# Performance work log

Measured on AMD Instinct MI355X. Metric: run time of the kernel, lower is better.

Reference implementation:

```python
import jax, jax.numpy as jnp
import numpy as np
import math

B = 50        # graphs per batch
NPG = 2000    # nodes per graph
EPG = 12000   # edges per graph
F_IN = 256
NHID = 128
RATIO = 0.8


def setup_inputs() -> dict:
    key = jax.random.key(0)
    ks = jax.random.split(key, 12)
    N = B * NPG
    src_loc = jax.random.randint(ks[0], (B, EPG), 0, NPG)
    dst_loc = jax.random.randint(ks[1], (B, EPG), 0, NPG)
    off = (jnp.arange(B) * NPG)[:, None]
    edge_index = jnp.stack([(src_loc + off).reshape(-1), (dst_loc + off).reshape(-1)]).astype(jnp.int32)

    def lin(k, fi, fo):
        return (jax.random.normal(k, (fi, fo), jnp.float32) / np.sqrt(fi).astype(np.float32))

    return {
        "x": jax.random.normal(ks[2], (N, F_IN), jnp.float32),
        "W1": lin(ks[3], F_IN, NHID), "b1": jnp.zeros(NHID, jnp.float32),
        "Ws1": lin(ks[4], NHID, 1), "bs1": jnp.zeros(1, jnp.float32),
        "W2": lin(ks[5], NHID, NHID), "b2": jnp.zeros(NHID, jnp.float32),
        "Ws2": lin(ks[6], NHID, 1), "bs2": jnp.zeros(1, jnp.float32),
        "W3": lin(ks[7], NHID, NHID), "b3": jnp.zeros(NHID, jnp.float32),
        "Ws3": lin(ks[8], NHID, 1), "bs3": jnp.zeros(1, jnp.float32),
        "Wl": lin(ks[9], 2 * NHID, NHID), "bl": jnp.zeros(NHID, jnp.float32),
        "edge_index": edge_index,
    }


def gcn_conv(x, W, b, src, dst, w, N):
    # PyG GCNConv: D^{-1/2} (A + I) D^{-1/2} X W + b, deg from edge weights + self loop
    h = x @ W
    deg = jax.ops.segment_sum(w, dst, num_segments=N) + 1.0
    dis = jax.lax.rsqrt(deg)
    norm = w * dis[src] * dis[dst]                       # [E]
    agg = jax.ops.segment_sum(h[src] * norm[:, None], dst, num_segments=N)
    return agg + h / deg[:, None] + b                    # self-loop norm = 1/deg


def sag_pool(x, src, dst, w, Ws, bs, n_per_graph):
    N = x.shape[0]
    k = math.ceil(RATIO * n_per_graph)
    score = gcn_conv(x, Ws, bs, src, dst, w, N)[:, 0]    # [N]
    _, topi = jax.lax.top_k(score.reshape(B, n_per_graph), k)
    perm = (topi + (jnp.arange(B) * n_per_graph)[:, None]).reshape(-1)
    x_new = x[perm] * jnp.tanh(score[perm])[:, None]
    # filter_adj: keep edges whose endpoints survive, reindex; dropped edges -> weight 0
    mapping = jnp.full((N,), -1, jnp.int32).at[perm].set(jnp.arange(B * k, dtype=jnp.int32))
    ns, nd = mapping[src], mapping[dst]
    valid = (ns >= 0) & (nd >= 0) & (w > 0)
    return (x_new, jnp.where(valid, ns, 0), jnp.where(valid, nd, 0),
            jnp.where(valid, w, jnp.zeros((), x.dtype)), k)


def readout(x, n):
    # global max pool || global mean pool (equal-size graphs, nodes grouped per graph)
    xr = x.reshape(B, n, -1)
    return jnp.concatenate([xr.max(axis=1), xr.mean(axis=1)], axis=-1)


def reference(x, W1, b1, Ws1, bs1, W2, b2, Ws2, bs2, W3, b3, Ws3, bs3, Wl, bl, edge_index):
    src, dst = edge_index[0], edge_index[1]
    w = jnp.ones(src.shape[0], x.dtype)
    n = NPG
    x = jax.nn.relu(gcn_conv(x, W1, b1, src, dst, w, B * n))
    x, src, dst, w, n = sag_pool(x, src, dst, w, Ws1, bs1, n)
    x1 = readout(x, n)
    x = jax.nn.relu(gcn_conv(x, W2, b2, src, dst, w, B * n))
    x, src, dst, w, n = sag_pool(x, src, dst, w, Ws2, bs2, n)
    x2 = readout(x, n)
    x = jax.nn.relu(gcn_conv(x, W3, b3, src, dst, w, B * n))
    x, src, dst, w, n = sag_pool(x, src, dst, w, Ws3, bs3, n)
    x3 = readout(x, n)
    return jax.nn.relu((x1 + x2 + x3) @ Wl + bl)
```

## Files before the change

kernel.cpp:

```cpp
#include <hip/hip_runtime.h>
#include <math.h>

#define B_GRAPHS 50
#define NPG0     2000
#define EPG      12000
#define F_IN_C   256
#define NHID     128
#define N0       (B_GRAPHS * NPG0)
#define NE       (B_GRAPHS * EPG)
#define RSEG     16
#define GSLOTS   7
#define CPAD     136

typedef _Float16 f16x8 __attribute__((ext_vector_type(8)));
typedef float    f32x4 __attribute__((ext_vector_type(4)));

static inline int cdiv(int a, int b) { return (a + b - 1) / b; }

__global__ void k_fill_start(int* __restrict__ cnt, float* __restrict__ accum) {
    int i = blockIdx.x * 256 + threadIdx.x;
    if (i < N0) cnt[i] = 0;
    if (i < B_GRAPHS * 256) accum[i] = 0.f;
}

__global__ void k_init_edges(const int* __restrict__ ei, int* __restrict__ esrc,
                             int* __restrict__ edst, float* __restrict__ ew,
                             int* __restrict__ cnt) {
    int e = blockIdx.x * 256 + threadIdx.x;
    if (e < NE) {
        int d = ei[NE + e];
        esrc[e] = ei[e]; edst[e] = d; ew[e] = 1.0f;
        atomicAdd(&cnt[d], 1);
    }
}

__global__ void k_cvt_all(const float* __restrict__ W1, const float* __restrict__ W2,
                          const float* __restrict__ W3, _Float16* __restrict__ WT1,
                          _Float16* __restrict__ WT2, _Float16* __restrict__ WT3) {
    int t = blockIdx.x * 256 + threadIdx.x;
    if (t < 128 * 256) {
        int n = t >> 8, kk = t & 255;
        WT1[t] = (_Float16)W1[kk * 128 + n];
    } else if (t < 128 * 256 + 128 * 128) {
        int u = t - 32768; int n = u >> 7, kk = u & 127;
        WT2[u] = (_Float16)W2[kk * 128 + n];
    } else {
        int u = t - 49152; int n = u >> 7, kk = u & 127;
        WT3[u] = (_Float16)W3[kk * 128 + n];
    }
}

template<int FP32IN, int F, int GATHER>
__global__ __launch_bounds__(256) void k_gemm_ws(const void* __restrict__ Xin,
                                                 const _Float16* __restrict__ WT,
                                                 const int* __restrict__ perm,
                                                 const float* __restrict__ gate,
                                                 _Float16* __restrict__ H, int N) {
    constexpr int KH  = (F > 128) ? 128 : F;
    constexpr int K8H = KH / 8;
    constexpr int SMEMSZ = (128 * KH > 128 * CPAD) ? 128 * KH : 128 * CPAD;
    __shared__ _Float16 smem[SMEMSZ];
    const int tid  = threadIdx.x;
    const int wave = tid >> 6, lane = tid & 63;
    const int quad = lane >> 4, l16 = lane & 15;
    const int m_blk = blockIdx.x * 128;

    f32x4 acc[2][8];
#pragma unroll
    for (int i = 0; i < 2; ++i)
#pragma unroll
        for (int j = 0; j < 8; ++j) acc[i][j] = {0.f, 0.f, 0.f, 0.f};

    int row0 = m_blk + wave * 32 + l16;
    int row1 = row0 + 16;
    if (row0 > N - 1) row0 = N - 1;
    if (row1 > N - 1) row1 = N - 1;
    _Float16 g0 = (_Float16)1.0f, g1 = (_Float16)1.0f;
    if (GATHER) {
        g0 = (_Float16)gate[row0]; g1 = (_Float16)gate[row1];
        row0 = perm[row0]; row1 = perm[row1];
    }
    const int sx = l16 & 7;
    constexpr int NKQ = F / 32;

    if (FP32IN) {
        constexpr int PD = (NKQ < 4) ? NKQ : 4;
        const float* base0 = (const float*)Xin + (size_t)row0 * F + quad * 8;
        const float* base1 = (const float*)Xin + (size_t)row1 * F + quad * 8;
        float4 p0[PD][2], p1[PD][2];
#pragma unroll
        for (int i = 0; i < PD; ++i) {
            p0[i][0] = ((const float4*)(base0 + i * 32))[0];
            p0[i][1] = ((const float4*)(base0 + i * 32))[1];
            p1[i][0] = ((const float4*)(base1 + i * 32))[0];
            p1[i][1] = ((const float4*)(base1 + i * 32))[1];
        }
#pragma unroll
        for (int c = tid; c < 128 * K8H; c += 256) {
            int n = c / K8H, k8 = c - n * K8H;
            f16x8 v = *(const f16x8*)&WT[(size_t)(n * (F / 8) + k8) * 8];
            *(f16x8*)&smem[n * KH + ((k8 ^ (n & 7)) << 3)] = v;
        }
        __syncthreads();
#pragma unroll
        for (int kq = 0; kq < NKQ; ++kq) {
            if (KH < F && kq == NKQ / 2) {
                __syncthreads();
#pragma unroll
                for (int c = tid; c < 128 * K8H; c += 256) {
                    int n = c / K8H, k8 = c - n * K8H;
                    f16x8 v = *(const f16x8*)&WT[(size_t)(n * (F / 8) + K8H + k8) * 8];
                    *(f16x8*)&smem[n * KH + ((k8 ^ (n & 7)) << 3)] = v;
                }
                __syncthreads();
            }
            const int b = kq % PD;
            float4 f0 = p0[b][0], f1 = p0[b][1], h0 = p1[b][0], h1 = p1[b][1];
            if (kq + PD < NKQ) {
                p0[b][0] = ((const float4*)(base0 + (kq + PD) * 32))[0];
                p0[b][1] = ((const float4*)(base0 + (kq + PD) * 32))[1];
                p1[b][0] = ((const float4*)(base1 + (kq + PD) * 32))[0];
                p1[b][1] = ((const float4*)(base1 + (kq + PD) * 32))[1];
            }
            f16x8 af0 = (f16x8){(_Float16)f0.x,(_Float16)f0.y,(_Float16)f0.z,(_Float16)f0.w,
                                (_Float16)f1.x,(_Float16)f1.y,(_Float16)f1.z,(_Float16)f1.w};
            f16x8 af1 = (f16x8){(_Float16)h0.x,(_Float16)h0.y,(_Float16)h0.z,(_Float16)h0.w,
                                (_Float16)h1.x,(_Float16)h1.y,(_Float16)h1.z,(_Float16)h1.w};
            f16x8 bf[8];
#pragma unroll
            for (int j = 0; j < 8; ++j)
                bf[j] = *(const f16x8*)&smem[(j * 16 + l16) * KH + (((((kq & 3) << 2) + quad) ^ sx) << 3)];
#pragma unroll
            for (int j = 0; j < 8; ++j) {
                acc[0][j] = __builtin_amdgcn_mfma_f32_16x16x32_f16(af0, bf[j], acc[0][j], 0, 0, 0);
                acc[1][j] = __builtin_amdgcn_mfma_f32_16x16x32_f16(af1, bf[j], acc[1][j], 0, 0, 0);
            }
        }
    } else {
#pragma unroll
        for (int c = tid; c < 128 * K8H; c += 256) {
            int n = c / K8H, k8 = c - n * K8H;
            f16x8 v = *(const f16x8*)&WT[(size_t)(n * K8H + k8) * 8];
            *(f16x8*)&smem[n * KH + ((k8 ^ (n & 7)) << 3)] = v;
        }
        const _Float16* base0 = (const _Float16*)Xin + (size_t)row0 * F + quad * 8;
        const _Float16* base1 = (const _Float16*)Xin + (size_t)row1 * F + quad * 8;
        f16x8 q0[NKQ], q1[NKQ];
#pragma unroll
        for (int i = 0; i < NKQ; ++i) {
            q0[i] = *(const f16x8*)(base0 + i * 32);
            q1[i] = *(const f16x8*)(base1 + i * 32);
        }
        __syncthreads();
#pragma unroll
        for (int kq = 0; kq < NKQ; ++kq) {
            f16x8 af0 = q0[kq], af1 = q1[kq];
            if (GATHER) { af0 = af0 * g0; af1 = af1 * g1; }
            f16x8 bf[8];
#pragma unroll
            for (int j = 0; j < 8; ++j)
                bf[j] = *(const f16x8*)&smem[(j * 16 + l16) * KH + (((((kq & 3) << 2) + quad) ^ sx) << 3)];
#pragma unroll
            for (int j = 0; j < 8; ++j) {
                acc[0][j] = __builtin_amdgcn_mfma_f32_16x16x32_f16(af0, bf[j], acc[0][j], 0, 0, 0);
                acc[1][j] = __builtin_amdgcn_mfma_f32_16x16x32_f16(af1, bf[j], acc[1][j], 0, 0, 0);
            }
        }
    }
    __syncthreads();

    _Float16* sC = smem;
    const int rw = wave * 32;
#pragma unroll
    for (int i = 0; i < 2; ++i)
#pragma unroll
        for (int j = 0; j < 8; ++j)
#pragma unroll
            for (int g = 0; g < 4; ++g)
                sC[(rw + i * 16 + quad * 4 + g) * CPAD + j * 16 + l16] = (_Float16)acc[i][j][g];
    __syncthreads();
    {
        int rr = tid >> 1;
        int gr = m_blk + rr;
        if (gr < N) {
            _Float16* Hr = H + (size_t)gr * 128 + (tid & 1) * 64;
            const _Float16* Sr = sC + rr * CPAD + (tid & 1) * 64;
#pragma unroll
            for (int c = 0; c < 8; ++c)
                *(f16x8*)&Hr[c * 8] = *(const f16x8*)&Sr[c * 8];
        }
    }
}

__global__ __launch_bounds__(256) void k_scan(const int* __restrict__ cnt,
                                              int* __restrict__ offs,
                                              int* __restrict__ cursor, int npg) {
    __shared__ int ch[256];
    int b = blockIdx.x, tid = threadIdx.x;
    int per = (npg + 255) >> 8;
    int base = b * npg;
    int s0 = tid * per;
    int s1 = s0 + per; if (s1 > npg) s1 = npg; if (s0 > npg) s0 = npg;
    int s = 0;
    for (int i = s0; i < s1; ++i) s += cnt[base + i];
    ch[tid] = s;
    __syncthreads();
    for (int d = 1; d < 256; d <<= 1) {
        int t = ch[tid] + ((tid >= d) ? ch[tid - d] : 0);
        __syncthreads();
        ch[tid] = t;
        __syncthreads();
    }
    int run = b * EPG + ch[tid] - s;
    for (int i = s0; i < s1; ++i) {
        offs[base + i] = run; cursor[base + i] = run;
        run += cnt[base + i];
    }
}

__global__ void k_fill_csr(const int* __restrict__ esrc, const int* __restrict__ edst,
                           const float* __restrict__ ew, const int* __restrict__ cnt,
                           int* __restrict__ cursor, int* __restrict__ csr_src,
                           float* __restrict__ csr_norm) {
    int e = blockIdx.x * 256 + threadIdx.x;
    if (e < NE) {
        if (ew[e] > 0.f) {
            int sN = esrc[e], d = edst[e];
            int pos = atomicAdd(&cursor[d], 1);
            csr_src[pos] = sN;
            csr_norm[pos] = rsqrtf((float)(cnt[sN] + 1)) * rsqrtf((float)(cnt[d] + 1));
        }
    }
}

__global__ __launch_bounds__(256) void k_agg(const _Float16* __restrict__ H,
                                             const int* __restrict__ csr_src,
                                             const float* __restrict__ csr_norm,
                                             const int* __restrict__ offs,
                                             const int* __restrict__ cnt,
                                             const float* __restrict__ bias,
                                             const float* __restrict__ Ws,
                                             _Float16* __restrict__ X,
                                             float* __restrict__ hs,
                                             int bpg, int npg) {
    int bi = blockIdx.x;
    int x = bi & 7, s = bi >> 3;
    int gslot = s / bpg, blk = s - gslot * bpg;
    int g = x + 8 * gslot;
    if (g >= B_GRAPHS) return;
    int node = g * npg + blk * 4 + (threadIdx.x >> 6);
    int lane = threadIdx.x & 63;
    int quad = lane >> 4, l16 = lane & 15;

    int st = offs[node], c = cnt[node], en = st + c;
    float acc[8];
#pragma unroll
    for (int j = 0; j < 8; ++j) acc[j] = 0.f;

    if (c > 0) {
        for (int e0 = st; e0 < en; e0 += 8) {
            int eA = e0 + quad, eB = eA + 4;
            int ecA = eA < en ? eA : en - 1;
            int ecB = eB < en ? eB : en - 1;
            int uA = csr_src[ecA], uB = csr_src[ecB];
            float nA = (eA < en) ? csr_norm[ecA] : 0.f;
            float nB = (eB < en) ? csr_norm[ecB] : 0.f;
            f16x8 hA = *(const f16x8*)&H[(size_t)uA * NHID + l16 * 8];
            f16x8 hB = *(const f16x8*)&H[(size_t)uB * NHID + l16 * 8];
#pragma unroll
            for (int j = 0; j < 8; ++j) acc[j] = fmaf((float)hA[j], nA, acc[j]);
#pragma unroll
            for (int j = 0; j < 8; ++j) acc[j] = fmaf((float)hB[j], nB, acc[j]);
        }
    }
#pragma unroll
    for (int j = 0; j < 8; ++j) {
        acc[j] += __shfl_xor(acc[j], 16, 64);
        acc[j] += __shfl_xor(acc[j], 32, 64);
    }
    float invd = 1.f / (float)(c + 1);
    f16x8 hn = *(const f16x8*)&H[(size_t)node * NHID + l16 * 8];
    float4 b0 = *(const float4*)&bias[l16 * 8];
    float4 b1 = *(const float4*)&bias[l16 * 8 + 4];
    float4 w0 = *(const float4*)&Ws[l16 * 8];
    float4 w1 = *(const float4*)&Ws[l16 * 8 + 4];
    const float bb[8] = {b0.x, b0.y, b0.z, b0.w, b1.x, b1.y, b1.z, b1.w};
    const float ww[8] = {w0.x, w0.y, w0.z, w0.w, w1.x, w1.y, w1.z, w1.w};
    float sd = 0.f;
    f16x8 o;
#pragma unroll
    for (int j = 0; j < 8; ++j) {
        float v = fmaxf(acc[j] + (float)hn[j] * invd + bb[j], 0.f);
        o[j] = (_Float16)v;
        sd = fmaf(v, ww[j], sd);
    }
    if (quad == 0)
        *(f16x8*)&X[(size_t)node * NHID + l16 * 8] = o;
    sd += __shfl_xor(sd, 1, 64);
    sd += __shfl_xor(sd, 2, 64);
    sd += __shfl_xor(sd, 4, 64);
    sd += __shfl_xor(sd, 8, 64);
    if (lane == 0) hs[node] = sd;
}

__global__ void k_score(const float* __restrict__ hs, const int* __restrict__ csr_src,
                        const float* __restrict__ csr_norm, const int* __restrict__ offs,
                        const int* __restrict__ cnt, const float* __restrict__ bs,
                        float* __restrict__ score, int N) {
    int i = blockIdx.x * 256 + threadIdx.x;
    if (i >= N) return;
    int s = offs[i], c = cnt[i];
    float a = 0.f;
    for (int e = s; e < s + c; ++e) a = fmaf(hs[csr_src[e]], csr_norm[e], a);
    score[i] = a + hs[i] / (float)(c + 1) + bs[0];
}

__global__ __launch_bounds__(1024) void k_topk(const float* __restrict__ score,
                                               int* __restrict__ mapping,
                                               int* __restrict__ perm,
                                               float* __restrict__ gate,
                                               int* __restrict__ cntN,
                                               int npg, int k) {
    __shared__ float ss[2048];
    __shared__ int   si[2048];
    int b = blockIdx.x, tid = threadIdx.x;
    for (int i = tid; i < 2048; i += 1024) {
        if (i < npg) { ss[i] = score[b * npg + i]; si[i] = i; }
        else         { ss[i] = -__builtin_inff();  si[i] = i; }
    }
    __syncthreads();
    for (int size = 2; size <= 2048; size <<= 1) {
        for (int stride = size >> 1; stride > 0; stride >>= 1) {
            int t = tid;
            int i = ((t & ~(stride - 1)) << 1) | (t & (stride - 1));
            int j = i | stride;
            float sa = ss[i], sb = ss[j];
            int   ia = si[i], ib = si[j];
            bool b_before_a = (sb > sa) || (sb == sa && ib < ia);
            bool forward = ((i & size) == 0);
            bool doswap = forward ? b_before_a : !b_before_a;
            if (doswap) { ss[i] = sb; ss[j] = sa; si[i] = ib; si[j] = ia; }
            __syncthreads();
        }
    }
    for (int j = tid; j < npg; j += 1024) {
        int oldg = b * npg + si[j];
        if (j < k) {
            int newg = b * k + j;
            perm[newg] = oldg;
            mapping[oldg] = newg;
            gate[newg] = tanhf(ss[j]);
        } else {
            mapping[oldg] = -1;
        }
    }
    for (int j = tid; j < k; j += 1024) cntN[b * k + j] = 0;
}

__global__ __launch_bounds__(128) void k_pool_readout(const _Float16* __restrict__ X,
                                                      const float* __restrict__ gate,
                                                      const int* __restrict__ perm,
                                                      float* __restrict__ pmax,
                                                      float* __restrict__ psum, int k) {
    int s = blockIdx.x, b = blockIdx.y, f = threadIdx.x;
    int j0 = (k * s) / RSEG, j1 = (k * (s + 1)) / RSEG;
    float mx = -__builtin_inff(), sm = 0.f;
    for (int j = j0; j < j1; ++j) {
        int g = b * k + j;
        int old = perm[g];
        float v = (float)X[(size_t)old * NHID + f] * gate[g];
        mx = fmaxf(mx, v);
        sm += v;
    }
    pmax[(size_t)(b * RSEG + s) * NHID + f] = mx;
    psum[(size_t)(b * RSEG + s) * NHID + f] = sm;
}

__global__ __launch_bounds__(128) void k_readout_comb(const float* __restrict__ pmax,
                                                      const float* __restrict__ psum,
                                                      float* __restrict__ accum, int k) {
    int b = blockIdx.x, f = threadIdx.x;
    float mx = -__builtin_inff(), sm = 0.f;
#pragma unroll
    for (int s = 0; s < RSEG; ++s) {
        mx = fmaxf(mx, pmax[(size_t)(b * RSEG + s) * NHID + f]);
        sm += psum[(size_t)(b * RSEG + s) * NHID + f];
    }
    accum[b * 256 + f]       += mx;
    accum[b * 256 + 128 + f] += sm / (float)k;
}

__global__ void k_remap(int* __restrict__ esrc, int* __restrict__ edst,
                        float* __restrict__ ew, const int* __restrict__ mapping,
                        int* __restrict__ cntN) {
    int e = blockIdx.x * 256 + threadIdx.x;
    if (e >= NE) return;
    int sN = esrc[e], d = edst[e];
    float we = ew[e];
    int ns = mapping[sN], nd = mapping[d];
    bool valid = (ns >= 0) && (nd >= 0) && (we > 0.f);
    esrc[e] = valid ? ns : 0;
    edst[e] = valid ? nd : 0;
    ew[e] = valid ? we : 0.f;
    if (valid) atomicAdd(&cntN[nd], 1);
}

__global__ __launch_bounds__(128) void k_comb_final(const float* __restrict__ pmax,
                                                    const float* __restrict__ psum,
                                                    const float* __restrict__ accum,
                                                    const float* __restrict__ Wl,
                                                    const float* __restrict__ bl,
                                                    float* __restrict__ out, int k) {
    __shared__ float a[256];
    int b = blockIdx.x, f = threadIdx.x;
    float mx = -__builtin_inff(), sm = 0.f;
#pragma unroll
    for (int s = 0; s < RSEG; ++s) {
        mx = fmaxf(mx, pmax[(size_t)(b * RSEG + s) * NHID + f]);
        sm += psum[(size_t)(b * RSEG + s) * NHID + f];
    }
    a[f]       = accum[b * 256 + f] + mx;
    a[128 + f] = accum[b * 256 + 128 + f] + sm / (float)k;
    __syncthreads();
    float s = bl[f];
    for (int i = 0; i < 256; ++i) s = fmaf(a[i], Wl[i * NHID + f], s);
    out[b * NHID + f] = fmaxf(s, 0.f);
}

extern "C" void kernel_launch(void* const* d_in, const int* in_sizes, int n_in,
                              void* d_out, int out_size, void* d_ws, size_t ws_size,
                              hipStream_t stream) {
    const float* x0 = (const float*)d_in[0];
    const float* Wm[3] = {(const float*)d_in[1], (const float*)d_in[5], (const float*)d_in[9]};
    const float* bm[3] = {(const float*)d_in[2], (const float*)d_in[6], (const float*)d_in[10]};
    const float* Wsc[3] = {(const float*)d_in[3], (const float*)d_in[7], (const float*)d_in[11]};
    const float* bsc[3] = {(const float*)d_in[4], (const float*)d_in[8], (const float*)d_in[12]};
    const float* Wl = (const float*)d_in[13];
    const float* bl = (const float*)d_in[14];
    const int*   ei = (const int*)d_in[15];
    float* out = (float*)d_out;

    _Float16* bufA = (_Float16*)d_ws;
    _Float16* bufB = bufA + (size_t)N0 * NHID;
    _Float16* WT1  = bufB + (size_t)N0 * NHID;
    _Float16* WT2  = WT1 + 128 * 256;
    _Float16* WT3  = WT2 + 128 * 128;
    float* hs     = (float*)(WT3 + 128 * 128);
    float* score  = hs + N0;
    float* gate   = score + N0;
    float* accum  = gate + N0;
    float* pmax   = accum + B_GRAPHS * 256;
    float* psum   = pmax + B_GRAPHS * RSEG * NHID;
    int*   cntA   = (int*)(psum + B_GRAPHS * RSEG * NHID);
    int*   cntB   = cntA + N0;
    int*   offs   = cntB + N0;
    int*   cursor = offs + N0;
    int*   mapping= cursor + N0;
    int*   perm   = mapping + N0;
    int*   esrc   = perm + N0;
    int*   edst   = esrc + NE;
    float* ew     = (float*)(edst + NE);
    int*   csr_src= (int*)(ew + NE);
    float* csr_norm = (float*)(csr_src + NE);

    _Float16* WTs[3] = {WT1, WT2, WT3};
    const int EG = cdiv(NE, 256);

    k_fill_start<<<cdiv(N0, 256), 256, 0, stream>>>(cntA, accum);
    k_init_edges<<<EG, 256, 0, stream>>>(ei, esrc, edst, ew, cntA);
    k_cvt_all<<<256, 256, 0, stream>>>(Wm[0], Wm[1], Wm[2], WT1, WT2, WT3);

    int npg = NPG0;
    _Float16* Hbuf = bufA; _Float16* Xbuf = bufB;

    for (int layer = 0; layer < 3; ++layer) {
        int N = B_GRAPHS * npg;
        int k = (npg * 4) / 5;
        int NG = cdiv(N, 256);
        int bpg = npg >> 2;
        int* cnt  = (layer == 1) ? cntB : cntA;
        int* cntN = (layer == 1) ? cntA : cntB;

        if (layer == 0)
            k_gemm_ws<1, 256, 0><<<cdiv(N, 128), 256, 0, stream>>>(x0, WTs[0], perm, gate, Hbuf, N);
        else
            k_gemm_ws<0, 128, 1><<<cdiv(N, 128), 256, 0, stream>>>(Xbuf, WTs[layer], perm, gate, Hbuf, N);
        k_scan<<<B_GRAPHS, 256, 0, stream>>>(cnt, offs, cursor, npg);
        k_fill_csr<<<EG, 256, 0, stream>>>(esrc, edst, ew, cnt, cursor, csr_src, csr_norm);
        k_agg<<<8 * GSLOTS * bpg, 256, 0, stream>>>(Hbuf, csr_src, csr_norm, offs, cnt,
                                                    bm[layer], Wsc[layer], Xbuf, hs, bpg, npg);
        k_score<<<NG, 256, 0, stream>>>(hs, csr_src, csr_norm, offs, cnt, bsc[layer], score, N);
        k_topk<<<B_GRAPHS, 1024, 0, stream>>>(score, mapping, perm, gate, cntN, npg, k);
        k_pool_readout<<<dim3(RSEG, B_GRAPHS), 128, 0, stream>>>(Xbuf, gate, perm, pmax, psum, k);
        if (layer < 2) {
            k_remap<<<EG, 256, 0, stream>>>(esrc, edst, ew, mapping, cntN);
            k_readout_comb<<<B_GRAPHS, 128, 0, stream>>>(pmax, psum, accum, k);
        } else {
            k_comb_final<<<B_GRAPHS, 128, 0, stream>>>(pmax, psum, accum, Wl, bl, out, k);
        }

        npg = k;
    }
}
```

Before: 639.7 us.

## Halve GEMM row tile, merge init kernels, and fuse readout into one kernel

The GEMM tile shrinks from 128 to 64 rows per block, with one 16-row MFMA strip per wave, which doubles the grid and lowers register pressure to raise occupancy. The edge-init and weight-conversion kernels are merged into a single launch. The two-pass pool readout (partial max/sum, then combine) becomes one 512-thread kernel per graph that reduces in shared memory and, on the last layer, also applies the final linear layer. This removes several launches and the partial buffers, but the readout now runs on only 50 blocks and each GEMM block reuses its loaded weights over fewer rows.

```diff
diff --git a/kernel.cpp b/kernel.cpp
--- a/kernel.cpp
+++ b/kernel.cpp
@@ -8,7 +8,6 @@
 #define NHID     128
 #define N0       (B_GRAPHS * NPG0)
 #define NE       (B_GRAPHS * EPG)
-#define RSEG     16
 #define GSLOTS   7
 #define CPAD     136
 
@@ -23,28 +22,25 @@
     if (i < B_GRAPHS * 256) accum[i] = 0.f;
 }
 
-__global__ void k_init_edges(const int* __restrict__ ei, int* __restrict__ esrc,
-                             int* __restrict__ edst, float* __restrict__ ew,
-                             int* __restrict__ cnt) {
-    int e = blockIdx.x * 256 + threadIdx.x;
-    if (e < NE) {
-        int d = ei[NE + e];
-        esrc[e] = ei[e]; edst[e] = d; ew[e] = 1.0f;
+__global__ void k_init_cvt(const int* __restrict__ ei, int* __restrict__ esrc,
+                           int* __restrict__ edst, float* __restrict__ ew,
+                           int* __restrict__ cnt,
+                           const float* __restrict__ W1, const float* __restrict__ W2,
+                           const float* __restrict__ W3, _Float16* __restrict__ WT1,
+                           _Float16* __restrict__ WT2, _Float16* __restrict__ WT3) {
+    int t = blockIdx.x * 256 + threadIdx.x;
+    if (t < NE) {
+        int d = ei[NE + t];
+        esrc[t] = ei[t]; edst[t] = d; ew[t] = 1.0f;
         atomicAdd(&cnt[d], 1);
     }
-}
-
-__global__ void k_cvt_all(const float* __restrict__ W1, const float* __restrict__ W2,
-                          const float* __restrict__ W3, _Float16* __restrict__ WT1,
-                          _Float16* __restrict__ WT2, _Float16* __restrict__ WT3) {
-    int t = blockIdx.x * 256 + threadIdx.x;
     if (t < 128 * 256) {
         int n = t >> 8, kk = t & 255;
         WT1[t] = (_Float16)W1[kk * 128 + n];
     } else if (t < 128 * 256 + 128 * 128) {
         int u = t - 32768; int n = u >> 7, kk = u & 127;
         WT2[u] = (_Float16)W2[kk * 128 + n];
-    } else {
+    } else if (t < 128 * 256 + 2 * 128 * 128) {
         int u = t - 49152; int n = u >> 7, kk = u & 127;
         WT3[u] = (_Float16)W3[kk * 128 + n];
     }
@@ -58,27 +54,23 @@
                                                  _Float16* __restrict__ H, int N) {
     constexpr int KH  = (F > 128) ? 128 : F;
     constexpr int K8H = KH / 8;
-    constexpr int SMEMSZ = (128 * KH > 128 * CPAD) ? 128 * KH : 128 * CPAD;
+    constexpr int SMEMSZ = (128 * KH > 64 * CPAD) ? 128 * KH : 64 * CPAD;
     __shared__ _Float16 smem[SMEMSZ];
     const int tid  = threadIdx.x;
     const int wave = tid >> 6, lane = tid & 63;
     const int quad = lane >> 4, l16 = lane & 15;
-    const int m_blk = blockIdx.x * 128;
-
-    f32x4 acc[2][8];
-#pragma unroll
-    for (int i = 0; i < 2; ++i)
-#pragma unroll
-        for (int j = 0; j < 8; ++j) acc[i][j] = {0.f, 0.f, 0.f, 0.f};
-
-    int row0 = m_blk + wave * 32 + l16;
-    int row1 = row0 + 16;
+    const int m_blk = blockIdx.x * 64;
+
+    f32x4 acc[8];
+#pragma unroll
+    for (int j = 0; j < 8; ++j) acc[j] = {0.f, 0.f, 0.f, 0.f};
+
+    int row0 = m_blk + wave * 16 + l16;
     if (row0 > N - 1) row0 = N - 1;
-    if (row1 > N - 1) row1 = N - 1;
-    _Float16 g0 = (_Float16)1.0f, g1 = (_Float16)1.0f;
+    _Float16 g0 = (_Float16)1.0f;
     if (GATHER) {
-        g0 = (_Float16)gate[row0]; g1 = (_Float16)gate[row1];
-        row0 = perm[row0]; row1 = perm[row1];
+        g0 = (_Float16)gate[row0];
+        row0 = perm[row0];
     }
     const int sx = l16 & 7;
     constexpr int NKQ = F / 32;
@@ -86,14 +78,11 @@
     if (FP32IN) {
         constexpr int PD = (NKQ < 4) ? NKQ : 4;
         const float* base0 = (const float*)Xin + (size_t)row0 * F + quad * 8;
-        const float* base1 = (const float*)Xin + (size_t)row1 * F + quad * 8;
-        float4 p0[PD][2], p1[PD][2];
+        float4 p0[PD][2];
 #pragma unroll
         for (int i = 0; i < PD; ++i) {
             p0[i][0] = ((const float4*)(base0 + i * 32))[0];
             p0[i][1] = ((const float4*)(base0 + i * 32))[1];
-            p1[i][0] = ((const float4*)(base1 + i * 32))[0];
-            p1[i][1] = ((const float4*)(base1 + i * 32))[1];
         }
 #pragma unroll
         for (int c = tid; c < 128 * K8H; c += 256) {
@@ -115,26 +104,20 @@
                 __syncthreads();
             }
             const int b = kq % PD;
-            float4 f0 = p0[b][0], f1 = p0[b][1], h0 = p1[b][0], h1 = p1[b][1];
+            float4 f0 = p0[b][0], f1 = p0[b][1];
             if (kq + PD < NKQ) {
                 p0[b][0] = ((const float4*)(base0 + (kq + PD) * 32))[0];
                 p0[b][1] = ((const float4*)(base0 + (kq + PD) * 32))[1];
-                p1[b][0] = ((const float4*)(base1 + (kq + PD) * 32))[0];
-                p1[b][1] = ((const float4*)(base1 + (kq + PD) * 32))[1];
             }
             f16x8 af0 = (f16x8){(_Float16)f0.x,(_Float16)f0.y,(_Float16)f0.z,(_Float16)f0.w,
                                 (_Float16)f1.x,(_Float16)f1.y,(_Float16)f1.z,(_Float16)f1.w};
-            f16x8 af1 = (f16x8){(_Float16)h0.x,(_Float16)h0.y,(_Float16)h0.z,(_Float16)h0.w,
-                                (_Float16)h1.x,(_Float16)h1.y,(_Float16)h1.z,(_Float16)h1.w};
             f16x8 bf[8];
 #pragma unroll
             for (int j = 0; j < 8; ++j)
                 bf[j] = *(const f16x8*)&smem[(j * 16 + l16) * KH + (((((kq & 3) << 2) + quad) ^ sx) << 3)];
 #pragma unroll
-            for (int j = 0; j < 8; ++j) {
-                acc[0][j] = __builtin_amdgcn_mfma_f32_16x16x32_f16(af0, bf[j], acc[0][j], 0, 0, 0);
-                acc[1][j] = __builtin_amdgcn_mfma_f32_16x16x32_f16(af1, bf[j], acc[1][j], 0, 0, 0);
-            }
+            for (int j = 0; j < 8; ++j)
+                acc[j] = __builtin_amdgcn_mfma_f32_16x16x32_f16(af0, bf[j], acc[j], 0, 0, 0);
         }
     } else {
 #pragma unroll
@@ -144,49 +127,43 @@
             *(f16x8*)&smem[n * KH + ((k8 ^ (n & 7)) << 3)] = v;
         }
         const _Float16* base0 = (const _Float16*)Xin + (size_t)row0 * F + quad * 8;
-        const _Float16* base1 = (const _Float16*)Xin + (size_t)row1 * F + quad * 8;
-        f16x8 q0[NKQ], q1[NKQ];
-#pragma unroll
-        for (int i = 0; i < NKQ; ++i) {
+        f16x8 q0[NKQ];
+#pragma unroll
+        for (int i = 0; i < NKQ; ++i)
             q0[i] = *(const f16x8*)(base0 + i * 32);
-            q1[i] = *(const f16x8*)(base1 + i * 32);
-        }
         __syncthreads();
 #pragma unroll
         for (int kq = 0; kq < NKQ; ++kq) {
-            f16x8 af0 = q0[kq], af1 = q1[kq];
-            if (GATHER) { af0 = af0 * g0; af1 = af1 * g1; }
+            f16x8 af0 = q0[kq];
+            if (GATHER) af0 = af0 * g0;
             f16x8 bf[8];
 #pragma unroll
             for (int j = 0; j < 8; ++j)
                 bf[j] = *(const f16x8*)&smem[(j * 16 + l16) * KH + (((((kq & 3) << 2) + quad) ^ sx) << 3)];
 #pragma unroll
-            for (int j = 0; j < 8; ++j) {
-                acc[0][j] = __builtin_amdgcn_mfma_f32_16x16x32_f16(af0, bf[j], acc[0][j], 0, 0, 0);
-                acc[1][j] = __builtin_amdgcn_mfma_f32_16x16x32_f16(af1, bf[j], acc[1][j], 0, 0, 0);
-            }
+            for (int j = 0; j < 8; ++j)
+                acc[j] = __builtin_amdgcn_mfma_f32_16x16x32_f16(af0, bf[j], acc[j], 0, 0, 0);
         }
     }
     __syncthreads();
 
     _Float16* sC = smem;
-    const int rw = wave * 32;
-#pragma unroll
-    for (int i = 0; i < 2; ++i)
-#pragma unroll
-        for (int j = 0; j < 8; ++j)
-#pragma unroll
-            for (int g = 0; g < 4; ++g)
-                sC[(rw + i * 16 + quad * 4 + g) * CPAD + j * 16 + l16] = (_Float16)acc[i][j][g];
+    const int rw = wave * 16;
+#pragma unroll
+    for (int j = 0; j < 8; ++j)
+#pragma unroll
+        for (int g = 0; g < 4; ++g)
+            sC[(rw + quad * 4 + g) * CPAD + j * 16 + l16] = (_Float16)acc[j][g];
     __syncthreads();
     {
-        int rr = tid >> 1;
+        int rr = tid >> 2;
+        int cc = (tid & 3) * 32;
         int gr = m_blk + rr;
         if (gr < N) {
-            _Float16* Hr = H + (size_t)gr * 128 + (tid & 1) * 64;
-            const _Float16* Sr = sC + rr * CPAD + (tid & 1) * 64;
-#pragma unroll
-            for (int c = 0; c < 8; ++c)
+            _Float16* Hr = H + (size_t)gr * 128 + cc;
+            const _Float16* Sr = sC + rr * CPAD + cc;
+#pragma unroll
+            for (int c = 0; c < 4; ++c)
                 *(f16x8*)&Hr[c * 8] = *(const f16x8*)&Sr[c * 8];
         }
     }
@@ -357,37 +334,51 @@
     for (int j = tid; j < k; j += 1024) cntN[b * k + j] = 0;
 }
 
-__global__ __launch_bounds__(128) void k_pool_readout(const _Float16* __restrict__ X,
-                                                      const float* __restrict__ gate,
-                                                      const int* __restrict__ perm,
-                                                      float* __restrict__ pmax,
-                                                      float* __restrict__ psum, int k) {
-    int s = blockIdx.x, b = blockIdx.y, f = threadIdx.x;
-    int j0 = (k * s) / RSEG, j1 = (k * (s + 1)) / RSEG;
+template<int FINAL>
+__global__ __launch_bounds__(512) void k_readout(const _Float16* __restrict__ X,
+                                                 const float* __restrict__ gate,
+                                                 const int* __restrict__ perm,
+                                                 float* __restrict__ accum,
+                                                 const float* __restrict__ Wl,
+                                                 const float* __restrict__ bl,
+                                                 float* __restrict__ out, int k) {
+    __shared__ float sred[8][128];
+    __shared__ float afin[256];
+    int b = blockIdx.x;
+    int f = threadIdx.x & 127, seg = threadIdx.x >> 7;
+    int q = k >> 2;
     float mx = -__builtin_inff(), sm = 0.f;
-    for (int j = j0; j < j1; ++j) {
-        int g = b * k + j;
-        int old = perm[g];
-        float v = (float)X[(size_t)old * NHID + f] * gate[g];
+    int g0 = b * k + seg * q;
+    for (int j = 0; j < q; ++j) {
+        int g = g0 + j;
+        float v = (float)X[(size_t)perm[g] * NHID + f] * gate[g];
         mx = fmaxf(mx, v);
         sm += v;
     }
-    pmax[(size_t)(b * RSEG + s) * NHID + f] = mx;
-    psum[(size_t)(b * RSEG + s) * NHID + f] = sm;
-}
-
-__global__ __launch_bounds__(128) void k_readout_comb(const float* __restrict__ pmax,
-                                                      const float* __restrict__ psum,
-                                                      float* __restrict__ accum, int k) {
-    int b = blockIdx.x, f = threadIdx.x;
-    float mx = -__builtin_inff(), sm = 0.f;
-#pragma unroll
-    for (int s = 0; s < RSEG; ++s) {
-        mx = fmaxf(mx, pmax[(size_t)(b * RSEG + s) * NHID + f]);
-        sm += psum[(size_t)(b * RSEG + s) * NHID + f];
-    }
-    accum[b * 256 + f]       += mx;
-    accum[b * 256 + 128 + f] += sm / (float)k;
+    sred[seg][f] = mx;
+    sred[4 + seg][f] = sm;
+    __syncthreads();
+    if (threadIdx.x < 128) {
+        float M = fmaxf(fmaxf(sred[0][f], sred[1][f]), fmaxf(sred[2][f], sred[3][f]));
+        float S = sred[4][f] + sred[5][f] + sred[6][f] + sred[7][f];
+        float aM = accum[b * 256 + f] + M;
+        float aS = accum[b * 256 + 128 + f] + S / (float)k;
+        if (!FINAL) {
+            accum[b * 256 + f] = aM;
+            accum[b * 256 + 128 + f] = aS;
+        } else {
+            afin[f] = aM;
+            afin[128 + f] = aS;
+        }
+    }
+    if (FINAL) {
+        __syncthreads();
+        if (threadIdx.x < 128) {
+            float s = bl[f];
+            for (int i = 0; i < 256; ++i) s = fmaf(afin[i], Wl[i * NHID + f], s);
+            out[b * NHID + f] = fmaxf(s, 0.f);
+        }
+    }
 }
 
 __global__ void k_remap(int* __restrict__ esrc, int* __restrict__ edst,
@@ -405,28 +396,6 @@
     if (valid) atomicAdd(&cntN[nd], 1);
 }
 
-__global__ __launch_bounds__(128) void k_comb_final(const float* __restrict__ pmax,
-                                                    const float* __restrict__ psum,
-                                                    const float* __restrict__ accum,
-                                                    const float* __restrict__ Wl,
-                                                    const float* __restrict__ bl,
-                                                    float* __restrict__ out, int k) {
-    __shared__ float a[256];
-    int b = blockIdx.x, f = threadIdx.x;
-    float mx = -__builtin_inff(), sm = 0.f;
-#pragma unroll
-    for (int s = 0; s < RSEG; ++s) {
-        mx = fmaxf(mx, pmax[(size_t)(b * RSEG + s) * NHID + f]);
-        sm += psum[(size_t)(b * RSEG + s) * NHID + f];
-    }
-    a[f]       = accum[b * 256 + f] + mx;
-    a[128 + f] = accum[b * 256 + 128 + f] + sm / (float)k;
-    __syncthreads();
-    float s = bl[f];
-    for (int i = 0; i < 256; ++i) s = fmaf(a[i], Wl[i * NHID + f], s);
-    out[b * NHID + f] = fmaxf(s, 0.f);
-}
-
 extern "C" void kernel_launch(void* const* d_in, const int* in_sizes, int n_in,
                               void* d_out, int out_size, void* d_ws, size_t ws_size,
                               hipStream_t stream) {
@@ -449,9 +418,7 @@
     float* score  = hs + N0;
     float* gate   = score + N0;
     float* accum  = gate + N0;
-    float* pmax   = accum + B_GRAPHS * 256;
-    float* psum   = pmax + B_GRAPHS * RSEG * NHID;
-    int*   cntA   = (int*)(psum + B_GRAPHS * RSEG * NHID);
+    int*   cntA   = (int*)(accum + B_GRAPHS * 256);
     int*   cntB   = cntA + N0;
     int*   offs   = cntB + N0;
     int*   cursor = offs + N0;
@@ -467,8 +434,8 @@
     const int EG = cdiv(NE, 256);
 
     k_fill_start<<<cdiv(N0, 256), 256, 0, stream>>>(cntA, accum);
-    k_init_edges<<<EG, 256, 0, stream>>>(ei, esrc, edst, ew, cntA);
-    k_cvt_all<<<256, 256, 0, stream>>>(Wm[0], Wm[1], Wm[2], WT1, WT2, WT3);
+    k_init_cvt<<<EG, 256, 0, stream>>>(ei, esrc, edst, ew, cntA,
+                                       Wm[0], Wm[1], Wm[2], WT1, WT2, WT3);
 
     int npg = NPG0;
     _Float16* Hbuf = bufA; _Float16* Xbuf = bufB;
@@ -482,21 +449,22 @@
         int* cntN = (layer == 1) ? cntA : cntB;
 
         if (layer == 0)
-            k_gemm_ws<1, 256, 0><<<cdiv(N, 128), 256, 0, stream>>>(x0, WTs[0], perm, gate, Hbuf, N);
+            k_gemm_ws<1, 256, 0><<<cdiv(N, 64), 256, 0, stream>>>(x0, WTs[0], perm, gate, Hbuf, N);
         else
-            k_gemm_ws<0, 128, 1><<<cdiv(N, 128), 256, 0, stream>>>(Xbuf, WTs[layer], perm, gate, Hbuf, N);
+            k_gemm_ws<0, 128, 1><<<cdiv(N, 64), 256, 0, stream>>>(Xbuf, WTs[layer], perm, gate, Hbuf, N);
         k_scan<<<B_GRAPHS, 256, 0, stream>>>(cnt, offs, cursor, npg);
         k_fill_csr<<<EG, 256, 0, stream>>>(esrc, edst, ew, cnt, cursor, csr_src, csr_norm);
         k_agg<<<8 * GSLOTS * bpg, 256, 0, stream>>>(Hbuf, csr_src, csr_norm, offs, cnt,
                                                     bm[layer], Wsc[layer], Xbuf, hs, bpg, npg);
         k_score<<<NG, 256, 0, stream>>>(hs, csr_src, csr_norm, offs, cnt, bsc[layer], score, N);
         k_topk<<<B_GRAPHS, 1024, 0, stream>>>(score, mapping, perm, gate, cntN, npg, k);
-        k_pool_readout<<<dim3(RSEG, B_GRAPHS), 128, 0, stream>>>(Xbuf, gate, perm, pmax, psum, k);
         if (layer < 2) {
             k_remap<<<EG, 256, 0, stream>>>(esrc, edst, ew, mapping, cntN);
-            k_readout_comb<<<B_GRAPHS, 128, 0, stream>>>(pmax, psum, accum, k);
+            k_readout<0><<<B_GRAPHS, 512, 0, stream>>>(Xbuf, gate, perm, accum,
+                                                       nullptr, nullptr, nullptr, k);
         } else {
-            k_comb_final<<<B_GRAPHS, 128, 0, stream>>>(pmax, psum, accum, Wl, bl, out, k);
+            k_readout<1><<<B_GRAPHS, 512, 0, stream>>>(Xbuf, gate, perm, accum,
+                                                       Wl, bl, out, k);
         }
 
         npg = k;
```

Result: slower. 1.058 ms (+65.4%).
